# Optimization experiments

Hardware: AMD Instinct MI355X
Metric: run time of the kernel (lower is better)

## Reference

```python
import jax, jax.numpy as jnp
import numpy as np
from jax import lax

FILTER_SIZE = 11
N_ITER = 5


def gaussian_kernel1d(inv_theta, spacing, size):
    # distances = spacing * [-(size//2) .. size//2]; zero out center tap
    d = spacing * jnp.arange(-(size // 2), size // 2 + 1, dtype=jnp.float32)
    k = jnp.exp(-(d * inv_theta) ** 2 / 2)
    return k.at[size // 2].set(0.0)


def conv_along_axis(x, kernel, axis):
    # x: (C, *spatial); 1D conv along `axis`, 'same' padding (kernel symmetric -> corr == conv)
    x = jnp.moveaxis(x, axis, -1)
    shp = x.shape
    x2 = x.reshape(-1, 1, shp[-1])  # (M, 1, L)
    K = kernel.shape[0]
    out = lax.conv_general_dilated(
        x2, kernel[None, None, :].astype(x2.dtype), (1,), [(K // 2, K // 2)],
        dimension_numbers=('NCH', 'OIH', 'NCH'))
    return jnp.moveaxis(out.reshape(shp), -1, axis)


def _gaussian_filter_single(xi, inv_theta, spacing):
    # xi: (C, H, W); separable gaussian with per-sample spacing
    for i in range(2):
        k = gaussian_kernel1d(inv_theta[i], spacing[i], FILTER_SIZE)
        xi = conv_along_axis(xi, k, i + 1)
    return xi


_smooth = jax.vmap(_gaussian_filter_single, in_axes=(0, None, 0))


def reference(x, spatial_spacings, smoothness_weight, inv_smoothness_theta):
    n_classes = x.shape[1]
    comp = -jnp.eye(n_classes, dtype=x.dtype)  # -(label_i == label_j)
    negative_unary = x
    for _ in range(N_ITER):
        p = jax.nn.softmax(x, axis=1)
        s = smoothness_weight * _smooth(p, inv_smoothness_theta, spatial_spacings)
        c = jnp.einsum('bchw,cd->bdhw', s, comp)
        x = negative_unary - c
    return jax.nn.log_softmax(x, axis=1)


def setup_inputs() -> dict:
    key = jax.random.key(0)
    k1, = jax.random.split(key, 1)
    B, C, H, W = 16, 16, 384, 384
    return {
        'x': jax.random.normal(k1, (B, C, H, W), dtype=jnp.float32),
        'spatial_spacings': jnp.ones((B, 2), dtype=jnp.float32),
        'smoothness_weight': jnp.asarray(1.0, dtype=jnp.float32),
        'inv_smoothness_theta': jnp.ones((2,), dtype=jnp.float32),
    }
```

## Files before the change

kernel.cpp:

```cpp
#include <hip/hip_runtime.h>
#include <hip/hip_bf16.h>
#include <utility>

#define BB 16
#define CC 16
#define HH 384
#define WW 384
#define HWSZ (HH*WW)
#define CHW (CC*HWSZ)
#define NPIX (BB*CHW)

#define FT 768
#define ROWS 12
#define HSEGS (HH/ROWS)
#define SROW 408

typedef unsigned short ushortT;
template<int N> using ic = std::integral_constant<int, N>;

__device__ __forceinline__ void unpk2(unsigned u, float& lo, float& hi) {
    union { unsigned u; float f; } a, b;
    a.u = u << 16; b.u = u & 0xFFFF0000u;
    lo = a.f; hi = b.f;
}
__device__ __forceinline__ unsigned pk2(float lo, float hi) {
    __hip_bfloat162 h = __float22bfloat162_rn(make_float2(lo, hi));
    union { __hip_bfloat162 h; unsigned u; } c; c.h = h;
    return c.u;
}
__device__ __forceinline__ void unpk8(const uint4& q, float* v) {
    unpk2(q.x, v[0], v[1]); unpk2(q.y, v[2], v[3]);
    unpk2(q.z, v[4], v[5]); unpk2(q.w, v[6], v[7]);
}
__device__ __forceinline__ uint4 pk8(const float* v) {
    uint4 q;
    q.x = pk2(v[0], v[1]); q.y = pk2(v[2], v[3]);
    q.z = pk2(v[4], v[5]); q.w = pk2(v[6], v[7]);
    return q;
}
template<int CTRL>
__device__ __forceinline__ float dpp_f(float x) {
    union { float f; int i; } c; c.f = x;
    union { int i; float f; } r;
    r.i = __builtin_amdgcn_update_dpp(0, c.i, CTRL, 0xF, 0xF, true);
    return r.f;
}

template<int MODE>
__global__ __launch_bounds__(FT, 3) void k_fused(
    const void* __restrict__ in0, const ushortT* __restrict__ x0b,
    void* __restrict__ outp, ushortT* __restrict__ x0b_out,
    const float* __restrict__ spacings, const float* __restrict__ invtheta,
    const float* __restrict__ swp)
{
    __shared__ ushortT xp[4][CC][SROW];
    __shared__ __align__(16) float l_lds[2][WW];

    const int t  = threadIdx.x;
    const int b  = blockIdx.y;
    const int h0 = blockIdx.x * ROWS;

    {
        const int buf = t / (CC * 12);
        const int rem = t - buf * (CC * 12);
        const int c = rem / 12, s = rem - (rem / 12) * 12;
        const int e = (s < 4) ? (2 * s) : (392 + 2 * (s - 4));
        *(unsigned*)&xp[buf][c][e] = 0u;
    }

    const float sw  = swp[0];
    const float sch = spacings[b * 2 + 0] * invtheta[0];
    const float scw = spacings[b * 2 + 1] * invtheta[1];
    float kh[5], kw[5];
#pragma unroll
    for (int j = 0; j < 5; ++j) {
        float dh = sch * (float)(j - 5); kh[j] = __expf(-0.5f * dh * dh);
        float dw = scw * (float)(j - 5); kw[j] = __expf(-0.5f * dw * dw);
    }

    const int ca = t / 48, ga = t - (t / 48) * 48;
    const int cp = t >> 2, qq = t & 3;

    const size_t cbase = (size_t)b * CHW + (size_t)ca * HWSZ + (size_t)ga * 8;
    const uint4 z4 = make_uint4(0u, 0u, 0u, 0u);

    float wf[12][8];
    if (MODE >= 1) {
        const ushortT* tin = (const ushortT*)in0;
#pragma unroll
        for (int s = 0; s < 12; ++s) {
            const int r = h0 - 5 + s;
            const uint4 q = ((unsigned)r < HH)
                ? *(const uint4*)(tin + cbase + (size_t)r * WW) : z4;
            unpk8(q, wf[s]);
        }
    }

    __syncthreads();

    auto B_row = [&](int buf, int r) {
        float xa[4], xb[4];
#pragma unroll
        for (int i = 0; i < 4; ++i) {
            const unsigned u = *(const unsigned*)&xp[buf][qq * 4 + i][8 + 2 * cp];
            unpk2(u, xa[i], xb[i]);
        }
        float m0 = fmaxf(fmaxf(xa[0], xa[1]), fmaxf(xa[2], xa[3]));
        float m1 = fmaxf(fmaxf(xb[0], xb[1]), fmaxf(xb[2], xb[3]));
        m0 = fmaxf(m0, dpp_f<0xB1>(m0)); m0 = fmaxf(m0, dpp_f<0x4E>(m0));
        m1 = fmaxf(m1, dpp_f<0xB1>(m1)); m1 = fmaxf(m1, dpp_f<0x4E>(m1));
        float e0[4], e1[4], s0 = 0.f, s1 = 0.f;
#pragma unroll
        for (int i = 0; i < 4; ++i) {
            e0[i] = __expf(xa[i] - m0); s0 += e0[i];
            e1[i] = __expf(xb[i] - m1); s1 += e1[i];
        }
        s0 += dpp_f<0xB1>(s0); s0 += dpp_f<0x4E>(s0);
        s1 += dpp_f<0xB1>(s1); s1 += dpp_f<0x4E>(s1);
        if (MODE <= 1) {
            const float i0 = 1.0f / s0, i1 = 1.0f / s1;
#pragma unroll
            for (int i = 0; i < 4; ++i)
                *(unsigned*)&xp[buf][qq * 4 + i][8 + 2 * cp] = pk2(e0[i] * i0, e1[i] * i1);
        } else {
            if (qq == 0) {
                l_lds[r][2 * cp]     = m0 + __logf(s0);
                l_lds[r][2 * cp + 1] = m1 + __logf(s1);
            }
        }
    };

    auto C_row = [&](int h, int buf, int r) {
        if (MODE <= 1) {
            const uint4 q0 = *(const uint4*)&xp[buf][ca][ga * 8];
            const uint4 q1 = *(const uint4*)&xp[buf][ca][ga * 8 + 8];
            const uint4 q2 = *(const uint4*)&xp[buf][ca][ga * 8 + 16];
            float w[24];
            unpk8(q0, w); unpk8(q1, w + 8); unpk8(q2, w + 16);
            float o[8];
#pragma unroll
            for (int k = 0; k < 8; ++k) {
                float a = 0.f;
#pragma unroll
                for (int j = 0; j < 5; ++j)
                    a = fmaf(kw[j], w[k + 3 + j] + w[k + 13 - j], a);
                o[k] = a;
            }
            *(uint4*)((ushortT*)outp + cbase + (size_t)h * WW) = pk8(o);
        } else {
            const uint4 xq = *(const uint4*)&xp[buf][ca][8 + ga * 8];
            float xv[8]; unpk8(xq, xv);
            const float4 l0 = *(const float4*)&l_lds[r][ga * 8];
            const float4 l1 = *(const float4*)&l_lds[r][ga * 8 + 4];
            float* op = (float*)outp + cbase + (size_t)h * WW;
            *(float4*)op       = make_float4(xv[0]-l0.x, xv[1]-l0.y, xv[2]-l0.z, xv[3]-l0.w);
            *(float4*)(op + 4) = make_float4(xv[4]-l1.x, xv[5]-l1.y, xv[6]-l1.z, xv[7]-l1.w);
        }
    };

    auto A_row = [&](auto K0c, int h, int buf, const uint4& uq) {
        constexpr int k0 = decltype(K0c)::value;
        float acc[8];
#pragma unroll
        for (int k = 0; k < 8; ++k) acc[k] = 0.f;
#pragma unroll
        for (int j = 0; j < 5; ++j) {
            constexpr int DUMMY = 0; (void)DUMMY;
            const int sa = (k0 + j) % 12;
            const int sb = (k0 + 10 - j) % 12;
            const float kj = kh[j];
#pragma unroll
            for (int k = 0; k < 8; ++k)
                acc[k] = fmaf(kj, wf[sa][k] + wf[sb][k], acc[k]);
        }
        float uu[8]; unpk8(uq, uu);
        float xv[8];
#pragma unroll
        for (int k = 0; k < 8; ++k) xv[k] = fmaf(sw, acc[k], uu[k]);
        *(uint4*)&xp[buf][ca][8 + ga * 8] = pk8(xv);
    };

    auto A_row_m0 = [&](int h, int buf) {
        const float* xf = (const float*)in0;
        const float4 A0 = *(const float4*)(xf + cbase + (size_t)h * WW);
        const float4 A1 = *(const float4*)(xf + cbase + (size_t)h * WW + 4);
        float v[8] = {A0.x, A0.y, A0.z, A0.w, A1.x, A1.y, A1.z, A1.w};
        const uint4 q = pk8(v);
        *(uint4*)(x0b_out + cbase + (size_t)h * WW) = q;
        *(uint4*)&xp[buf][ca][8 + ga * 8] = q;
    };

    auto pair_body = [&](auto Pc) {
        constexpr int p = decltype(Pc)::value;
        const int h  = h0 + 2 * p;
        constexpr int bA = 2 * (p & 1);
        constexpr int bC = 2 * ((p & 1) ^ 1);

        if (MODE == 0) {
            if (p > 0) { C_row(h - 2, bC, 0); C_row(h - 1, bC + 1, 1); }
            A_row_m0(h, bA); A_row_m0(h + 1, bA + 1);
        } else {
            const ushortT* tin = (const ushortT*)in0;
            const uint4 uq0 = *(const uint4*)(x0b + cbase + (size_t)h * WW);
            const uint4 uq1 = *(const uint4*)(x0b + cbase + (size_t)(h + 1) * WW);
            uint4 nt0 = z4, nt1 = z4;
            if (p < 5) {
                const int r0 = h + 7, r1 = h + 8;
                if (r0 < HH) nt0 = *(const uint4*)(tin + cbase + (size_t)r0 * WW);
                if (r1 < HH) nt1 = *(const uint4*)(tin + cbase + (size_t)r1 * WW);
            }
            if (p > 0) { C_row(h - 2, bC, 0); C_row(h - 1, bC + 1, 1); }
            A_row(ic<2 * p>{},     h,     bA,     uq0);
            A_row(ic<2 * p + 1>{}, h + 1, bA + 1, uq1);
            if (p < 5) {
                unpk8(nt0, wf[(2 * p) % 12]);
                unpk8(nt1, wf[(2 * p + 1) % 12]);
            }
        }
        __syncthreads();
        B_row(bA, 0);
        B_row(bA + 1, 1);
        __syncthreads();
    };

    pair_body(ic<0>{}); pair_body(ic<1>{}); pair_body(ic<2>{});
    pair_body(ic<3>{}); pair_body(ic<4>{}); pair_body(ic<5>{});

    C_row(h0 + 10, 2, 0);
    C_row(h0 + 11, 3, 1);
}

extern "C" void kernel_launch(void* const* d_in, const int* in_sizes, int n_in,
                              void* d_out, int out_size, void* d_ws, size_t ws_size,
                              hipStream_t stream)
{
    const float* x0   = (const float*)d_in[0];
    const float* spac = (const float*)d_in[1];
    const float* sw   = (const float*)d_in[2];
    const float* it   = (const float*)d_in[3];

    ushortT* tA  = (ushortT*)d_ws;
    ushortT* tB  = tA + (size_t)NPIX;
    ushortT* x0b = tB + (size_t)NPIX;
    float*   out = (float*)d_out;

    dim3 gf(HSEGS, BB);
    dim3 bf(FT);

    k_fused<0><<<gf, bf, 0, stream>>>(x0, nullptr, tA, x0b, spac, it, sw);
    k_fused<1><<<gf, bf, 0, stream>>>(tA, x0b, tB, nullptr, spac, it, sw);
    k_fused<1><<<gf, bf, 0, stream>>>(tB, x0b, tA, nullptr, spac, it, sw);
    k_fused<1><<<gf, bf, 0, stream>>>(tA, x0b, tB, nullptr, spac, it, sw);
    k_fused<1><<<gf, bf, 0, stream>>>(tB, x0b, tA, nullptr, spac, it, sw);
    k_fused<2><<<gf, bf, 0, stream>>>(tA, x0b, out, nullptr, spac, it, sw);
}
```

Before: 436.3 us.

## Split width into strips with halo, shrink blocks to 224 threads

Tiles the width dimension into four 96-column strips, each block holding an 8-column halo on both sides and recomputing the softmax for the halo columns. Block size drops from 768 to 224 threads and LDS per block shrinks, so more blocks fit per CU. The 12-row vertical window is now kept packed as bf16 uint4 and unpacked when used, which cuts register pressure. In exchange, halo columns are loaded and computed redundantly (112 of every 96 useful columns), and some threads sit idle during the output phase.

After: 918.1 us. 2.1x slower.

```diff
diff --git a/kernel.cpp b/kernel.cpp
--- a/kernel.cpp
+++ b/kernel.cpp
@@ -10,10 +10,14 @@
 #define CHW (CC*HWSZ)
 #define NPIX (BB*CHW)
 
-#define FT 768
+#define FT 224
 #define ROWS 12
 #define HSEGS (HH/ROWS)
-#define SROW 408
+#define NSTRIP 4
+#define SWOUT 96
+#define SG 14
+#define SGO 12
+#define PLW 120
 
 typedef unsigned short ushortT;
 template<int N> using ic = std::integral_constant<int, N>;
@@ -47,26 +51,19 @@
 }
 
 template<int MODE>
-__global__ __launch_bounds__(FT, 3) void k_fused(
+__global__ __launch_bounds__(FT, 4) void k_fused(
     const void* __restrict__ in0, const ushortT* __restrict__ x0b,
     void* __restrict__ outp, ushortT* __restrict__ x0b_out,
     const float* __restrict__ spacings, const float* __restrict__ invtheta,
     const float* __restrict__ swp)
 {
-    __shared__ ushortT xp[4][CC][SROW];
-    __shared__ __align__(16) float l_lds[2][WW];
+    __shared__ ushortT xp[4][CC][PLW];
+    __shared__ float l_lds[4][112];
 
     const int t  = threadIdx.x;
-    const int b  = blockIdx.y;
+    const int b  = blockIdx.z;
     const int h0 = blockIdx.x * ROWS;
-
-    {
-        const int buf = t / (CC * 12);
-        const int rem = t - buf * (CC * 12);
-        const int c = rem / 12, s = rem - (rem / 12) * 12;
-        const int e = (s < 4) ? (2 * s) : (392 + 2 * (s - 4));
-        *(unsigned*)&xp[buf][c][e] = 0u;
-    }
+    const int W0 = blockIdx.y * SWOUT;
 
     const float sw  = swp[0];
     const float sch = spacings[b * 2 + 0] * invtheta[0];
@@ -78,31 +75,73 @@
         float dw = scw * (float)(j - 5); kw[j] = __expf(-0.5f * dw * dw);
     }
 
-    const int ca = t / 48, ga = t - (t / 48) * 48;
-    const int cp = t >> 2, qq = t & 3;
-
-    const size_t cbase = (size_t)b * CHW + (size_t)ca * HWSZ + (size_t)ga * 8;
+    const int ca = t / SG,  ga = t - (t / SG) * SG;
+    const int cp = t >> 2,  qq = t & 3;
+    const int co = t / SGO, go = t - (t / SGO) * SGO;
+    const bool cAct = (t < CC * SGO);
+
+    const int  gw    = W0 - 8 + ga * 8;
+    const bool colOK = ((unsigned)gw < WW);
+    const long long cbase = (long long)(b * CC + ca) * HWSZ + gw;
     const uint4 z4 = make_uint4(0u, 0u, 0u, 0u);
 
-    float wf[12][8];
-    if (MODE >= 1) {
+    uint4 win[12];
+    if constexpr (MODE >= 1) {
         const ushortT* tin = (const ushortT*)in0;
 #pragma unroll
         for (int s = 0; s < 12; ++s) {
             const int r = h0 - 5 + s;
-            const uint4 q = ((unsigned)r < HH)
-                ? *(const uint4*)(tin + cbase + (size_t)r * WW) : z4;
-            unpk8(q, wf[s]);
+            win[s] = (colOK && (unsigned)r < HH)
+                ? *(const uint4*)(tin + cbase + (long long)r * WW) : z4;
         }
     }
 
-    __syncthreads();
-
-    auto B_row = [&](int buf, int r) {
+    auto A_conv = [&](auto K0c, int buf, const uint4& uq) {
+        constexpr int k0 = decltype(K0c)::value;
+        float acc[8];
+#pragma unroll
+        for (int k = 0; k < 8; ++k) acc[k] = 0.f;
+#pragma unroll
+        for (int j = 0; j < 5; ++j) {
+            constexpr int dummy = 0; (void)dummy;
+            const int sa = (k0 + j) % 12;
+            const int sb = (k0 + 10 - j) % 12;
+            float e1[8], e2[8];
+            unpk8(win[sa], e1); unpk8(win[sb], e2);
+            const float kj = kh[j];
+#pragma unroll
+            for (int k = 0; k < 8; ++k) acc[k] = fmaf(kj, e1[k] + e2[k], acc[k]);
+        }
+        float uu[8]; unpk8(uq, uu);
+        float xv[8];
+#pragma unroll
+        for (int k = 0; k < 8; ++k) xv[k] = fmaf(sw, acc[k], uu[k]);
+        *(uint4*)&xp[buf][ca][ga * 8] = pk8(xv);
+    };
+
+    auto A_m0 = [&](int h, int buf) {
+        const float* xf = (const float*)in0;
+        float v[8];
+        if (colOK) {
+            const float4 A0 = *(const float4*)(xf + cbase + (long long)h * WW);
+            const float4 A1 = *(const float4*)(xf + cbase + (long long)h * WW + 4);
+            v[0]=A0.x; v[1]=A0.y; v[2]=A0.z; v[3]=A0.w;
+            v[4]=A1.x; v[5]=A1.y; v[6]=A1.z; v[7]=A1.w;
+        } else {
+#pragma unroll
+            for (int k = 0; k < 8; ++k) v[k] = 0.f;
+        }
+        const uint4 q = pk8(v);
+        if (ga >= 1 && ga <= SGO)
+            *(uint4*)(x0b_out + cbase + (long long)h * WW) = q;
+        *(uint4*)&xp[buf][ca][ga * 8] = q;
+    };
+
+    auto B_row = [&](int buf) {
         float xa[4], xb[4];
 #pragma unroll
         for (int i = 0; i < 4; ++i) {
-            const unsigned u = *(const unsigned*)&xp[buf][qq * 4 + i][8 + 2 * cp];
+            const unsigned u = *(const unsigned*)&xp[buf][qq * 4 + i][2 * cp];
             unpk2(u, xa[i], xb[i]);
         }
         float m0 = fmaxf(fmaxf(xa[0], xa[1]), fmaxf(xa[2], xa[3]));
@@ -117,24 +156,25 @@
         }
         s0 += dpp_f<0xB1>(s0); s0 += dpp_f<0x4E>(s0);
         s1 += dpp_f<0xB1>(s1); s1 += dpp_f<0x4E>(s1);
-        if (MODE <= 1) {
-            const float i0 = 1.0f / s0, i1 = 1.0f / s1;
+        if constexpr (MODE <= 1) {
+            const float i0 = ((unsigned)(W0 - 8 + 2 * cp)     < WW) ? 1.0f / s0 : 0.f;
+            const float i1 = ((unsigned)(W0 - 8 + 2 * cp + 1) < WW) ? 1.0f / s1 : 0.f;
 #pragma unroll
             for (int i = 0; i < 4; ++i)
-                *(unsigned*)&xp[buf][qq * 4 + i][8 + 2 * cp] = pk2(e0[i] * i0, e1[i] * i1);
+                *(unsigned*)&xp[buf][qq * 4 + i][2 * cp] = pk2(e0[i] * i0, e1[i] * i1);
         } else {
             if (qq == 0) {
-                l_lds[r][2 * cp]     = m0 + __logf(s0);
-                l_lds[r][2 * cp + 1] = m1 + __logf(s1);
+                l_lds[buf][2 * cp]     = m0 + __logf(s0);
+                l_lds[buf][2 * cp + 1] = m1 + __logf(s1);
             }
         }
     };
 
-    auto C_row = [&](int h, int buf, int r) {
-        if (MODE <= 1) {
-            const uint4 q0 = *(const uint4*)&xp[buf][ca][ga * 8];
-            const uint4 q1 = *(const uint4*)&xp[buf][ca][ga * 8 + 8];
-            const uint4 q2 = *(const uint4*)&xp[buf][ca][ga * 8 + 16];
+    auto C_row = [&](int h, int buf) {
+        if constexpr (MODE <= 1) {
+            const uint4 q0 = *(const uint4*)&xp[buf][co][go * 8];
+            const uint4 q1 = *(const uint4*)&xp[buf][co][go * 8 + 8];
+            const uint4 q2 = *(const uint4*)&xp[buf][co][go * 8 + 16];
             float w[24];
             unpk8(q0, w); unpk8(q1, w + 8); unpk8(q2, w + 16);
             float o[8];
@@ -146,88 +186,54 @@
                     a = fmaf(kw[j], w[k + 3 + j] + w[k + 13 - j], a);
                 o[k] = a;
             }
-            *(uint4*)((ushortT*)outp + cbase + (size_t)h * WW) = pk8(o);
-        } else {
-            const uint4 xq = *(const uint4*)&xp[buf][ca][8 + ga * 8];
+            *(uint4*)((ushortT*)outp + (long long)(b * CC + co) * HWSZ
+                      + (long long)h * WW + W0 + go * 8) = pk8(o);
+        } else {
+            const uint4 xq = *(const uint4*)&xp[buf][co][8 + go * 8];
             float xv[8]; unpk8(xq, xv);
-            const float4 l0 = *(const float4*)&l_lds[r][ga * 8];
-            const float4 l1 = *(const float4*)&l_lds[r][ga * 8 + 4];
-            float* op = (float*)outp + cbase + (size_t)h * WW;
+            const float4 l0 = *(const float4*)&l_lds[buf][8 + go * 8];
+            const float4 l1 = *(const float4*)&l_lds[buf][8 + go * 8 + 4];
+            float* op = (float*)outp + (long long)(b * CC + co) * HWSZ
+                        + (long long)h * WW + W0 + go * 8;
             *(float4*)op       = make_float4(xv[0]-l0.x, xv[1]-l0.y, xv[2]-l0.z, xv[3]-l0.w);
             *(float4*)(op + 4) = make_float4(xv[4]-l1.x, xv[5]-l1.y, xv[6]-l1.z, xv[7]-l1.w);
         }
     };
 
-    auto A_row = [&](auto K0c, int h, int buf, const uint4& uq) {
-        constexpr int k0 = decltype(K0c)::value;
-        float acc[8];
-#pragma unroll
-        for (int k = 0; k < 8; ++k) acc[k] = 0.f;
-#pragma unroll
-        for (int j = 0; j < 5; ++j) {
-            constexpr int DUMMY = 0; (void)DUMMY;
-            const int sa = (k0 + j) % 12;
-            const int sb = (k0 + 10 - j) % 12;
-            const float kj = kh[j];
-#pragma unroll
-            for (int k = 0; k < 8; ++k)
-                acc[k] = fmaf(kj, wf[sa][k] + wf[sb][k], acc[k]);
-        }
-        float uu[8]; unpk8(uq, uu);
-        float xv[8];
-#pragma unroll
-        for (int k = 0; k < 8; ++k) xv[k] = fmaf(sw, acc[k], uu[k]);
-        *(uint4*)&xp[buf][ca][8 + ga * 8] = pk8(xv);
-    };
-
-    auto A_row_m0 = [&](int h, int buf) {
-        const float* xf = (const float*)in0;
-        const float4 A0 = *(const float4*)(xf + cbase + (size_t)h * WW);
-        const float4 A1 = *(const float4*)(xf + cbase + (size_t)h * WW + 4);
-        float v[8] = {A0.x, A0.y, A0.z, A0.w, A1.x, A1.y, A1.z, A1.w};
-        const uint4 q = pk8(v);
-        *(uint4*)(x0b_out + cbase + (size_t)h * WW) = q;
-        *(uint4*)&xp[buf][ca][8 + ga * 8] = q;
-    };
-
     auto pair_body = [&](auto Pc) {
         constexpr int p = decltype(Pc)::value;
-        const int h  = h0 + 2 * p;
+        const int h = h0 + 2 * p;
         constexpr int bA = 2 * (p & 1);
-        constexpr int bC = 2 * ((p & 1) ^ 1);
-
-        if (MODE == 0) {
-            if (p > 0) { C_row(h - 2, bC, 0); C_row(h - 1, bC + 1, 1); }
-            A_row_m0(h, bA); A_row_m0(h + 1, bA + 1);
+        constexpr int bC = bA ^ 2;
+
+        if constexpr (MODE == 0) {
+            if (p > 0 && cAct) { C_row(h - 2, bC); C_row(h - 1, bC | 1); }
+            A_m0(h, bA); A_m0(h + 1, bA | 1);
         } else {
             const ushortT* tin = (const ushortT*)in0;
-            const uint4 uq0 = *(const uint4*)(x0b + cbase + (size_t)h * WW);
-            const uint4 uq1 = *(const uint4*)(x0b + cbase + (size_t)(h + 1) * WW);
+            const uint4 uq0 = colOK ? *(const uint4*)(x0b + cbase + (long long)h * WW) : z4;
+            const uint4 uq1 = colOK ? *(const uint4*)(x0b + cbase + (long long)(h + 1) * WW) : z4;
             uint4 nt0 = z4, nt1 = z4;
             if (p < 5) {
                 const int r0 = h + 7, r1 = h + 8;
-                if (r0 < HH) nt0 = *(const uint4*)(tin + cbase + (size_t)r0 * WW);
-                if (r1 < HH) nt1 = *(const uint4*)(tin + cbase + (size_t)r1 * WW);
+                if (colOK && r0 < HH) nt0 = *(const uint4*)(tin + cbase + (long long)r0 * WW);
+                if (colOK && r1 < HH) nt1 = *(const uint4*)(tin + cbase + (long long)r1 * WW);
             }
-            if (p > 0) { C_row(h - 2, bC, 0); C_row(h - 1, bC + 1, 1); }
-            A_row(ic<2 * p>{},     h,     bA,     uq0);
-            A_row(ic<2 * p + 1>{}, h + 1, bA + 1, uq1);
-            if (p < 5) {
-                unpk8(nt0, wf[(2 * p) % 12]);
-                unpk8(nt1, wf[(2 * p + 1) % 12]);
-            }
+            if (p > 0 && cAct) { C_row(h - 2, bC); C_row(h - 1, bC | 1); }
+            A_conv(ic<(2 * p) % 12>{},     bA,     uq0);
+            A_conv(ic<(2 * p + 1) % 12>{}, bA | 1, uq1);
+            if (p < 5) { win[(2 * p) % 12] = nt0; win[(2 * p + 1) % 12] = nt1; }
         }
         __syncthreads();
-        B_row(bA, 0);
-        B_row(bA + 1, 1);
+        B_row(bA);
+        B_row(bA | 1);
         __syncthreads();
     };
 
     pair_body(ic<0>{}); pair_body(ic<1>{}); pair_body(ic<2>{});
     pair_body(ic<3>{}); pair_body(ic<4>{}); pair_body(ic<5>{});
 
-    C_row(h0 + 10, 2, 0);
-    C_row(h0 + 11, 3, 1);
+    if (cAct) { C_row(h0 + 10, 2); C_row(h0 + 11, 3); }
 }
 
 extern "C" void kernel_launch(void* const* d_in, const int* in_sizes, int n_in,
@@ -244,7 +250,7 @@
     ushortT* x0b = tB + (size_t)NPIX;
     float*   out = (float*)d_out;
 
-    dim3 gf(HSEGS, BB);
+    dim3 gf(HSEGS, NSTRIP, BB);
     dim3 bf(FT);
 
     k_fused<0><<<gf, bf, 0, stream>>>(x0, nullptr, tA, x0b, spac, it, sw);
```
